# Kernel optimization log

Measured on AMD Instinct MI355X. Metric: run time of the kernel, lower is better.

The kernel has to match this reference:

```python
import jax, jax.numpy as jnp
import numpy as np

B, S, D = 128, 50, 128
NUM_NODE = 40000
HOP, N_ITER, SAMPLE = 2, 2, 12
N_NEI = 8
TEMP, MU, LEAK = 0.5, 0.1, 0.2


def setup_inputs() -> dict:
    key = jax.random.key(0)
    ks = jax.random.split(key, 32)
    stdv = 1.0 / np.sqrt(D)
    u = lambda k, shp: jax.random.uniform(k, shp, jnp.float32, -stdv, stdv)
    return {
        "inputs": jax.random.randint(ks[0], (B, S), 0, NUM_NODE),
        "adj": jax.random.randint(ks[1], (B, S, S), 0, 5),
        "item": jax.random.randint(ks[2], (B, S), 0, NUM_NODE),
        "simi_mask": jax.random.randint(ks[3], (B, S, S), 0, 2),
        "as_items_0": jax.random.randint(ks[4], (B, S, N_NEI), 0, NUM_NODE),
        "as_items_1": jax.random.randint(ks[5], (B, S, N_NEI), 0, NUM_NODE),
        "as_items_ssl_0": jax.random.randint(ks[6], (B, S, N_NEI), 0, NUM_NODE),
        "as_items_ssl_1": jax.random.randint(ks[7], (B, S, N_NEI), 0, NUM_NODE),
        "last_item_mask": jnp.zeros((B, S), bool).at[:, -1].set(True),
        "adj_all": jax.random.randint(ks[8], (NUM_NODE, SAMPLE), 0, NUM_NODE),
        "num": jax.random.uniform(ks[9], (NUM_NODE, SAMPLE)),
        "emb": u(ks[10], (NUM_NODE, D)),
        "pos_emb": u(ks[11], (200, D)),
        "a_local": u(ks[12], (N_ITER, 4, D)),
        "mir_w1": u(ks[13], (N_ITER, D, D)),
        "mir_w2": u(ks[14], (N_ITER, D, D)),
        "glob_w1": u(ks[15], (HOP, D + 1, D)),
        "glob_w2": u(ks[16], (HOP, D, 1)),
        "glob_w3": u(ks[17], (HOP, 2 * D, D)),
        "attr_w": u(ks[18], (2 * D, D)),
        "highway_w": u(ks[19], (2 * D, D)),
        "glu1_w": u(ks[20], (D, D)),
        "glu2_w": u(ks[21], (D, D)),
        "glu4_w": u(ks[22], (D, D)),
        "glu4_b": u(ks[23], (D,)),
        "w_s": u(ks[24], (D, 1)),
        "gate_w": u(ks[25], (2 * D, D)),
    }


def _forward(num, emb, pos_emb, a_local, mir_w1, mir_w2, glob_w1, glob_w2, glob_w3,
             attr_w, highway_w, glu1_w, glu2_w, glu4_w, glu4_b, w_s, gate_w,
             inputs, adj, item, simi_mask, as_lists, as_ssl_lists, last_item_mask, adj_all):
    mi = (inputs != 0).astype(emb.dtype)  # [B,S]
    h = emb[inputs]                        # [B,S,D]

    # ---- AttributeAggregator (masked-mean pool per attribute + gated fusion) ----
    def pool(idx_list):
        ps = []
        for idx in idx_list:
            m = (idx != 0).astype(emb.dtype)[..., None]  # [B,S,N,1]
            ps.append(jnp.sum(emb[idx] * m, 2) / (jnp.sum(m, 2) + 1e-8))
        return jnp.mean(jnp.stack(ps), 0)  # [B,S,D]
    hf1 = pool(as_lists)
    hf2 = pool(as_ssl_lists)
    g_attr = jax.nn.sigmoid(jnp.concatenate([h, hf1], -1) @ attr_w)
    hf = g_attr * h + (1.0 - g_attr) * hf1

    # ---- multi-hop neighbor sampling (irregular gathers) ----
    neigh = [inputs]
    wts = []
    for _ in range(HOP):
        flat = neigh[-1].reshape(-1)
        neigh.append(adj_all[flat].reshape(B, -1))
        wts.append(num[flat].reshape(B, -1))
    ev = [emb[n] for n in neigh]  # [B,S,D], [B,S*12,D], [B,S*144,D]

    item_emb = emb[item] * mi[..., None]
    sess = jnp.sum(item_emb, 1) / jnp.sum(mi, -1, keepdims=True)  # [B,D]

    # ---- GlobalAggregator stack (GCE-GNN style attention over sampled neighbors) ----
    for n_hop in range(HOP):
        nxt = []
        for hop in range(HOP - n_hop):
            sv = ev[hop]                                   # [B,M,D]
            nv = ev[hop + 1].reshape(B, -1, SAMPLE, D)     # [B,M,12,D]
            nw = wts[hop].reshape(B, -1, SAMPLE)           # [B,M,12]
            extra = jnp.broadcast_to(sess[:, None, None, :], nv.shape)
            a = jnp.concatenate([extra * nv, nw[..., None]], -1)  # [B,M,12,D+1]
            a = jax.nn.leaky_relu(a @ glob_w1[n_hop], LEAK)
            a = jax.nn.softmax((a @ glob_w2[n_hop])[..., 0], -1)[..., None]
            agg = jnp.sum(a * nv, -2)
            nxt.append(jnp.tanh(jnp.concatenate([sv, agg], -1) @ glob_w3[n_hop]))
        ev = nxt
    h_global = ev[0].reshape(B, S, D)

    # ---- LocalAggregator (edge-typed GAT) + MirrorAggregator (gated exchange) ----
    x = h
    mirror = hf
    for i in range(HOP):
        e = jax.nn.leaky_relu(jnp.einsum('bid,bjd,kd->kbij', x, x, a_local[i]), LEAK)
        att = jnp.full((B, S, S), -9e15, x.dtype)
        for k in range(4):
            att = jnp.where(adj == k + 1, e[k], att)
        x = jax.nn.softmax(att, -1) @ x
        gm = jax.nn.sigmoid(x @ mir_w1[i] + mirror @ mir_w2[i])
        x, mirror = gm * x + (1.0 - gm) * mirror, gm * mirror + (1.0 - gm) * x

    # ---- highway + last-item select ----
    g = jax.nn.sigmoid(jnp.concatenate([h, x], -1) @ highway_w)
    x_dot = g * h + (1.0 - g) * x
    h_local = jnp.sum(x_dot * last_item_mask[..., None].astype(x_dot.dtype), 1)  # [B,D]

    mask = mi[..., None]
    pos = pos_emb[:S][None]  # [1,S,D]
    bw = emb[1:]             # [NUM_NODE-1,D]
    hs = jnp.sum(h_global * mask, -2) / jnp.sum(mask, 1)  # [B,D]

    # ---- SSL pairwise similarity loss ----
    sim = jnp.einsum('bid,bjd->bij', hf1, hf2) / TEMP
    l = -jnp.log(jax.nn.softmax(sim, 2) + 1e-8)
    simi_loss = jnp.mean(jnp.sum(l * (simi_mask == 1), (1, 2)))

    # ---- attention-style GLU scoring ----
    hp = x_dot + pos
    nh = jax.nn.sigmoid(hp @ glu1_w + hs[:, None, :] @ glu2_w + h_local[:, None, :] @ glu4_w + glu4_b)
    beta = (nh @ w_s) * mask
    zg = jnp.sum(beta * hp, 1)  # [B,D]
    gf = jax.nn.sigmoid(jnp.concatenate([zg, h_local], -1) @ gate_w) * MU
    zh = gf * h_local + (1.0 - gf) * zg
    scores = zh @ bw.T  # [B, NUM_NODE-1]
    return simi_loss, scores


def reference(inputs, adj, item, simi_mask, as_items_0, as_items_1,
              as_items_ssl_0, as_items_ssl_1, last_item_mask, adj_all, num,
              emb, pos_emb, a_local, mir_w1, mir_w2, glob_w1, glob_w2, glob_w3,
              attr_w, highway_w, glu1_w, glu2_w, glu4_w, glu4_b, w_s, gate_w):
    return _forward(num, emb, pos_emb, a_local, mir_w1, mir_w2, glob_w1, glob_w2, glob_w3,
                    attr_w, highway_w, glu1_w, glu2_w, glu4_w, glu4_b, w_s, gate_w,
                    inputs, adj, item, simi_mask, [as_items_0, as_items_1],
                    [as_items_ssl_0, as_items_ssl_1], last_item_mask, adj_all)
```

## Files before the change

### kernel.cpp

```cpp
#include <hip/hip_runtime.h>
#include <hip/hip_bf16.h>


#define B 128
#define S 50
#define D 128
#define SAMPLE 12
#define NNEI 8
#define NODES 40000
#define NSC (NODES - 1)
#define LEAK 0.2f
#define TEMPV 0.5f
#define MUV 0.1f
#define NEG_BIG -3.0e38f

typedef const float* fpp;
typedef float* fpw;
typedef unsigned short u16;
typedef __attribute__((ext_vector_type(8))) short bfrag8;
typedef __attribute__((ext_vector_type(4))) float f32x4;

__device__ __forceinline__ float sigm(float x) { return 1.f / (1.f + __expf(-x)); }
__device__ __forceinline__ float tanh_f(float x) { return 1.f - 2.f / (__expf(2.f * x) + 1.f); }
__device__ __forceinline__ float leaky(float x) { return x >= 0.f ? x : LEAK * x; }
__device__ __forceinline__ u16 f2bf(float v) {
  __hip_bfloat16 h = __float2bfloat16(v);
  return *reinterpret_cast<u16*>(&h);
}

__global__ __launch_bounds__(256) void kprep4(fpp gw1, fpp gw3,
                                              u16* __restrict__ p1a,
                                              u16* __restrict__ p1b,
                                              u16* __restrict__ p3a,
                                              u16* __restrict__ p3b) {
  int i = blockIdx.x * 256 + threadIdx.x;
  fpp W; u16* dst; int KS;
  if (i < 16384)      { W = gw1;             dst = p1a; KS = 4; }
  else if (i < 32768) { W = gw1 + 129 * 128; dst = p1b; KS = 4; i -= 16384; }
  else if (i < 65536) { W = gw3;             dst = p3a; KS = 8; i -= 32768; }
  else                { W = gw3 + 256 * 128; dst = p3b; KS = 8; i -= 65536; }
  int e = i & 7;
  int lane = (i >> 3) & 63;
  int rest = i >> 9;
  int ks = rest % KS, nt = rest / KS;
  int k = ks * 32 + ((lane >> 4) << 3) + e;
  int n = (nt << 4) + (lane & 15);
  dst[i] = f2bf(W[(long)k * 128 + n]);
}

__global__ __launch_bounds__(128) void k1_gather(
    const int* __restrict__ inputs, const int* __restrict__ as0,
    const int* __restrict__ as1, const int* __restrict__ ss0,
    const int* __restrict__ ss1, fpp emb, fpp attr_w,
    fpw h, fpw hf1, fpw hf2, float* __restrict__ mi, fpw xA, fpw mir) {
  int bs = blockIdx.x;
  int d = threadIdx.x;
  __shared__ float h_s[D], hf1_s[D];
  int inp = inputs[bs];
  float hv = emb[(long)inp * D + d];
  const int* lists[4] = {as0, as1, ss0, ss1};
  float p[4];
#pragma unroll
  for (int l = 0; l < 4; l++) {
    float sum = 0.f, cnt = 0.f;
    const int* L = lists[l] + (long)bs * NNEI;
#pragma unroll
    for (int n = 0; n < NNEI; n++) {
      int idx = L[n];
      if (idx != 0) { sum += emb[(long)idx * D + d]; cnt += 1.f; }
    }
    p[l] = sum / (cnt + 1e-8f);
  }
  float hf1v = 0.5f * (p[0] + p[1]);
  float hf2v = 0.5f * (p[2] + p[3]);
  h_s[d] = hv;
  hf1_s[d] = hf1v;
  __syncthreads();
  float acc = 0.f;
  for (int k = 0; k < D; k++)
    acc += h_s[k] * attr_w[(long)k * D + d] + hf1_s[k] * attr_w[(long)(D + k) * D + d];
  float g = sigm(acc);
  float hfv = g * hv + (1.f - g) * hf1v;
  long o = (long)bs * D + d;
  h[o] = hv; hf1[o] = hf1v; hf2[o] = hf2v; xA[o] = hv; mir[o] = hfv;
  if (d == 0) mi[bs] = (inp != 0) ? 1.f : 0.f;
}

__global__ __launch_bounds__(128) void k2_sess(const int* __restrict__ inputs,
                                               const int* __restrict__ item,
                                               fpp emb, fpw sess) {
  int b = blockIdx.x;
  int d = threadIdx.x;
  float acc = 0.f, ms = 0.f;
  for (int s = 0; s < S; s++) {
    int inp = inputs[b * S + s];
    float m = (inp != 0) ? 1.f : 0.f;
    int it = item[b * S + s];
    acc += emb[(long)it * D + d] * m;
    ms += m;
  }
  sess[(long)b * D + d] = acc / ms;
}

__global__ __launch_bounds__(256) void kG_global(
    const int* __restrict__ inputs, const int* __restrict__ adj_all,
    fpp num, fpp emb, fpp sess,
    fpp W1a, fpp W2a, fpp W1b, fpp W2b, fpp W3b,
    const u16* __restrict__ p1a, const u16* __restrict__ p1b,
    const u16* __restrict__ p3a, const u16* __restrict__ p3b,
    fpw hg) {
  int bs = blockIdx.x;
  int b = bs / S;
  int d = threadIdx.x;
  int lane = d & 63;
  int w = d >> 6;
  int p = w >> 1;
  int wp = w & 1;
  int c = d & 127;
  int q = lane >> 4;
  int mrow = lane & 15;

  __shared__ __align__(16) u16 nvs_l[2][16 * 136];
  __shared__ __align__(16) u16 svagg_l[16 * 264];
  __shared__ __align__(16) float ev_l[13 * 128];
  __shared__ __align__(16) float agg1_l[128];
  __shared__ float red_l[2][2][16];
  __shared__ float nw_l[2][16];
  __shared__ int n1_l[SAMPLE];

#pragma unroll
  for (int r = 12; r < 16; r++) {
    if (d < 136) { nvs_l[0][r * 136 + d] = 0; nvs_l[1][r * 136 + d] = 0; }
  }
#pragma unroll
  for (int r = 13; r < 16; r++) {
    svagg_l[r * 264 + d] = 0;
    if (d < 8) svagg_l[r * 264 + 256 + d] = 0;
  }

  float sess_c = sess[(long)b * D + c];
  int src0 = __builtin_amdgcn_readfirstlane(inputs[bs]);
  if (d < 128) svagg_l[0 * 264 + d] = f2bf(emb[(long)src0 * D + d]);
  if (d < SAMPLE) n1_l[d] = adj_all[(long)src0 * SAMPLE + d];

  float w2A[4], wlA[4], w2B[4], wlB[4];
#pragma unroll
  for (int nt = 0; nt < 4; nt++) {
    int colA = (wp * 4 + nt) * 16 + mrow;
    w2A[nt] = W2a[colA];
    wlA[nt] = W1a[(long)D * D + colA];
    int colB = (w * 4 + nt) * 16 + mrow;
    if (w < 2) { w2B[nt] = W2b[colB]; wlB[nt] = W1b[(long)D * D + colB]; }
  }
  __syncthreads();

  float pre_raw[SAMPLE];
  float pre_nw = 0.f;
  {
    int u0 = p * 7;
    int srcp = (u0 == 0) ? src0 : __builtin_amdgcn_readfirstlane(n1_l[u0 - 1]);
#pragma unroll
    for (int j = 0; j < SAMPLE; j++) {
      int nj = __builtin_amdgcn_readfirstlane(adj_all[(long)srcp * SAMPLE + j]);
      pre_raw[j] = emb[(long)nj * D + c];
    }
    if (c < SAMPLE) pre_nw = num[(long)srcp * SAMPLE + c];
  }
  for (int i = 0; i < 7; i++) {
    int u = p * 7 + i;
    bool act = (u < 13);
    float raw[SAMPLE];
    if (act) {
#pragma unroll
      for (int j = 0; j < SAMPLE; j++) {
        raw[j] = pre_raw[j];
        nvs_l[p][j * 136 + c] = f2bf(raw[j] * sess_c);
      }
      if (c < SAMPLE) nw_l[p][c] = pre_nw;
      if (u == 0) {
#pragma unroll
        for (int j = 0; j < SAMPLE; j++)
          svagg_l[(1 + j) * 264 + c] = f2bf(raw[j]);
      }
    }
    __syncthreads();
    if (i < 6 && (u + 1) < 13) {
      int srcn = __builtin_amdgcn_readfirstlane(n1_l[u]);
#pragma unroll
      for (int j = 0; j < SAMPLE; j++) {
        int nj = __builtin_amdgcn_readfirstlane(adj_all[(long)srcn * SAMPLE + j]);
        pre_raw[j] = emb[(long)nj * D + c];
      }
      if (c < SAMPLE) pre_nw = num[(long)srcn * SAMPLE + c];
    }
    if (act) {
      f32x4 acc[4];
#pragma unroll
      for (int nt = 0; nt < 4; nt++) acc[nt] = (f32x4){0.f, 0.f, 0.f, 0.f};
#pragma unroll
      for (int ks = 0; ks < 4; ks++) {
        bfrag8 a = *(const bfrag8*)(nvs_l[p] + mrow * 136 + q * 8 + ks * 32);
#pragma unroll
        for (int nt = 0; nt < 4; nt++) {
          bfrag8 bb = *(const bfrag8*)(p1a + ((wp * 4 + nt) * 4 + ks) * 512 + lane * 8);
          acc[nt] = __builtin_amdgcn_mfma_f32_16x16x32_bf16(a, bb, acc[nt], 0, 0, 0);
        }
      }
      float lp[4] = {0.f, 0.f, 0.f, 0.f};
      float nwq[4];
#pragma unroll
      for (int i2 = 0; i2 < 4; i2++) nwq[i2] = (q < 3) ? nw_l[p][q * 4 + i2] : 0.f;
#pragma unroll
      for (int nt = 0; nt < 4; nt++)
#pragma unroll
        for (int i2 = 0; i2 < 4; i2++)
          lp[i2] += leaky(acc[nt][i2] + nwq[i2] * wlA[nt]) * w2A[nt];
#pragma unroll
      for (int off = 1; off <= 8; off <<= 1)
#pragma unroll
        for (int i2 = 0; i2 < 4; i2++) lp[i2] += __shfl_xor(lp[i2], off, 64);
      if (mrow == 0 && q < 3) {
#pragma unroll
        for (int i2 = 0; i2 < 4; i2++) red_l[p][wp][q * 4 + i2] = lp[i2];
      }
    }
    __syncthreads();
    if (act) {
      float lg[SAMPLE];
#pragma unroll
      for (int j = 0; j < SAMPLE; j++) lg[j] = red_l[p][0][j] + red_l[p][1][j];
      float mx = lg[0];
#pragma unroll
      for (int j = 1; j < SAMPLE; j++) mx = fmaxf(mx, lg[j]);
      float se = 0.f;
#pragma unroll
      for (int j = 0; j < SAMPLE; j++) { lg[j] = __expf(lg[j] - mx); se += lg[j]; }
      float inv = 1.f / se;
      float aggd = 0.f;
#pragma unroll
      for (int j = 0; j < SAMPLE; j++) aggd += lg[j] * inv * raw[j];
      svagg_l[u * 264 + 128 + c] = f2bf(aggd);
    }
  }
  __syncthreads();

  {
    f32x4 accB[2];
#pragma unroll
    for (int nt = 0; nt < 2; nt++) accB[nt] = (f32x4){0.f, 0.f, 0.f, 0.f};
#pragma unroll
    for (int ks = 0; ks < 8; ks++) {
      bfrag8 a = *(const bfrag8*)(svagg_l + mrow * 264 + q * 8 + ks * 32);
#pragma unroll
      for (int nt = 0; nt < 2; nt++) {
        bfrag8 bb = *(const bfrag8*)(p3a + ((w * 2 + nt) * 8 + ks) * 512 + lane * 8);
        accB[nt] = __builtin_amdgcn_mfma_f32_16x16x32_bf16(a, bb, accB[nt], 0, 0, 0);
      }
    }
#pragma unroll
    for (int nt = 0; nt < 2; nt++) {
      int col = (w * 2 + nt) * 16 + mrow;
#pragma unroll
      for (int i2 = 0; i2 < 4; i2++) {
        int u2 = q * 4 + i2;
        if (u2 < 13) ev_l[u2 * 128 + col] = tanh_f(accB[nt][i2]);
      }
    }
  }
  __syncthreads();

  float evreg[SAMPLE];
  if (p == 0) {
#pragma unroll
    for (int j = 0; j < SAMPLE; j++) {
      float e = ev_l[(1 + j) * 128 + c];
      evreg[j] = e;
      nvs_l[0][j * 136 + c] = f2bf(e * sess_c);
    }
    if (c < SAMPLE) nw_l[0][c] = num[(long)src0 * SAMPLE + c];
  }
  __syncthreads();
  if (w < 2) {
    f32x4 acc[4];
#pragma unroll
    for (int nt = 0; nt < 4; nt++) acc[nt] = (f32x4){0.f, 0.f, 0.f, 0.f};
#pragma unroll
    for (int ks = 0; ks < 4; ks++) {
      bfrag8 a = *(const bfrag8*)(nvs_l[0] + mrow * 136 + q * 8 + ks * 32);
#pragma unroll
      for (int nt = 0; nt < 4; nt++) {
        bfrag8 bb = *(const bfrag8*)(p1b + ((w * 4 + nt) * 4 + ks) * 512 + lane * 8);
        acc[nt] = __builtin_amdgcn_mfma_f32_16x16x32_bf16(a, bb, acc[nt], 0, 0, 0);
      }
    }
    float lp[4] = {0.f, 0.f, 0.f, 0.f};
    float nwq[4];
#pragma unroll
    for (int i2 = 0; i2 < 4; i2++) nwq[i2] = (q < 3) ? nw_l[0][q * 4 + i2] : 0.f;
#pragma unroll
    for (int nt = 0; nt < 4; nt++)
#pragma unroll
      for (int i2 = 0; i2 < 4; i2++)
        lp[i2] += leaky(acc[nt][i2] + nwq[i2] * wlB[nt]) * w2B[nt];
#pragma unroll
    for (int off = 1; off <= 8; off <<= 1)
#pragma unroll
      for (int i2 = 0; i2 < 4; i2++) lp[i2] += __shfl_xor(lp[i2], off, 64);
    if (mrow == 0 && q < 3) {
#pragma unroll
      for (int i2 = 0; i2 < 4; i2++) red_l[0][w][q * 4 + i2] = lp[i2];
    }
  }
  __syncthreads();
  if (p == 0) {
    float lg[SAMPLE];
#pragma unroll
    for (int j = 0; j < SAMPLE; j++) lg[j] = red_l[0][0][j] + red_l[0][1][j];
    float mx = lg[0];
#pragma unroll
    for (int j = 1; j < SAMPLE; j++) mx = fmaxf(mx, lg[j]);
    float se = 0.f;
#pragma unroll
    for (int j = 0; j < SAMPLE; j++) { lg[j] = __expf(lg[j] - mx); se += lg[j]; }
    float inv = 1.f / se;
    float agg1d = 0.f;
#pragma unroll
    for (int j = 0; j < SAMPLE; j++) agg1d += lg[j] * inv * evreg[j];
    agg1_l[c] = agg1d;
  }
  __syncthreads();
  if (d < 128) {
    float accf = 0.f;
#pragma unroll 4
    for (int k4 = 0; k4 < 32; k4++) {
      float4 a4 = *(const float4*)&ev_l[4 * k4];
      float4 g4 = *(const float4*)&agg1_l[4 * k4];
      accf += a4.x * W3b[(4 * k4 + 0) * D + d] + a4.y * W3b[(4 * k4 + 1) * D + d] +
              a4.z * W3b[(4 * k4 + 2) * D + d] + a4.w * W3b[(4 * k4 + 3) * D + d] +
              g4.x * W3b[(D + 4 * k4 + 0) * D + d] + g4.y * W3b[(D + 4 * k4 + 1) * D + d] +
              g4.z * W3b[(D + 4 * k4 + 2) * D + d] + g4.w * W3b[(D + 4 * k4 + 3) * D + d];
    }
    hg[(long)bs * D + d] = tanh_f(accf);
  }
}

__global__ __launch_bounds__(128) void k5ab(fpp x, const int* __restrict__ adj,
                                            fpp a_loc, fpp w1, fpp w2,
                                            fpw xout, fpw mir,
                                            fpp hw, fpp h, fpw x_dot,
                                            float* __restrict__ h_local,
                                            int fin) {
  int b = blockIdx.x / S;
  int row = blockIdx.x % S;
  int tid = threadIdx.x;
  __shared__ float xi_s[D];
  __shared__ float ak_s[4][D];
  __shared__ float alpha_s[S];
  long idx = ((long)b * S + row) * D + tid;
  xi_s[tid] = x[idx];
#pragma unroll
  for (int k = 0; k < 4; k++) ak_s[k][tid] = a_loc[(long)k * D + tid];
  __syncthreads();
  if (tid < 64) {
    int j = tid;
    float att;
    if (j < S) {
      float acc0 = 0.f, acc1 = 0.f, acc2 = 0.f, acc3 = 0.f;
      const float* xj = x + ((long)b * S + j) * D;
      for (int dd = 0; dd < D; dd++) {
        float prod = xi_s[dd] * xj[dd];
        acc0 += prod * ak_s[0][dd];
        acc1 += prod * ak_s[1][dd];
        acc2 += prod * ak_s[2][dd];
        acc3 += prod * ak_s[3][dd];
      }
      int av = adj[((long)b * S + row) * S + j];
      att = -9e15f;
      if (av == 1) att = leaky(acc0);
      else if (av == 2) att = leaky(acc1);
      else if (av == 3) att = leaky(acc2);
      else if (av == 4) att = leaky(acc3);
    } else {
      att = NEG_BIG;
    }
    float mx = att;
#pragma unroll
    for (int o = 32; o > 0; o >>= 1) mx = fmaxf(mx, __shfl_xor(mx, o, 64));
    float e = __expf(att - mx);
    float ssum = e;
#pragma unroll
    for (int o = 32; o > 0; o >>= 1) ssum += __shfl_xor(ssum, o, 64);
    if (j < S) alpha_s[j] = e / ssum;
  }
  __syncthreads();
  float xn = 0.f;
  for (int j = 0; j < S; j++) xn += alpha_s[j] * x[((long)b * S + j) * D + tid];
  float mv = mir[idx];
  ak_s[0][tid] = xn;
  ak_s[1][tid] = mv;
  __syncthreads();
  float a2 = 0.f;
  for (int k = 0; k < D; k++)
    a2 += ak_s[0][k] * w1[(long)k * D + tid] + ak_s[1][k] * w2[(long)k * D + tid];
  float g = sigm(a2);
  float xg = g * xn + (1.f - g) * mv;
  if (!fin) {
    xout[idx] = xg;
    mir[idx] = g * mv + (1.f - g) * xn;
    return;
  }
  float hv = h[idx];
  ak_s[2][tid] = hv;
  ak_s[3][tid] = xg;
  __syncthreads();
  float a3 = 0.f;
  for (int k = 0; k < D; k++)
    a3 += ak_s[2][k] * hw[(long)k * D + tid] + ak_s[3][k] * hw[(long)(D + k) * D + tid];
  float gh = sigm(a3);
  float xd = gh * hv + (1.f - gh) * xg;
  x_dot[idx] = xd;
  if (row == S - 1) h_local[(long)b * D + tid] = xd;
}

__global__ __launch_bounds__(64) void k7_simi(fpp hf1, fpp hf2,
                                              const int* __restrict__ simi_mask,
                                              float* __restrict__ loss) {
  int b = blockIdx.x / S;
  int i = blockIdx.x % S;
  int j = threadIdx.x;
  __shared__ float hi_s[D];
  hi_s[j] = hf1[((long)b * S + i) * D + j];
  hi_s[j + 64] = hf1[((long)b * S + i) * D + j + 64];
  __syncthreads();
  float sim;
  if (j < S) {
    float acc = 0.f;
    const float* r = hf2 + ((long)b * S + j) * D;
    for (int dd = 0; dd < D; dd++) acc += hi_s[dd] * r[dd];
    sim = acc * (1.0f / TEMPV);
  } else {
    sim = NEG_BIG;
  }
  float mx = sim;
#pragma unroll
  for (int o = 32; o > 0; o >>= 1) mx = fmaxf(mx, __shfl_xor(mx, o, 64));
  float e = __expf(sim - mx);
  float ssum = e;
#pragma unroll
  for (int o = 32; o > 0; o >>= 1) ssum += __shfl_xor(ssum, o, 64);
  float contrib = 0.f;
  if (j < S) {
    float p = e / ssum;
    float l = -__logf(p + 1e-8f);
    if (simi_mask[((long)b * S + i) * S + j] == 1) contrib = l;
  }
#pragma unroll
  for (int o = 32; o > 0; o >>= 1) contrib += __shfl_xor(contrib, o, 64);
  if (j == 0) atomicAdd(loss, contrib);
}

__global__ __launch_bounds__(512) void k8_glu(
    fpp hg, fpp x_dot, fpp pos, fpp h_local, const float* __restrict__ mi,
    fpp glu1, fpp glu2, fpp glu4, fpp glu4b, fpp w_s, fpp gate_w, fpw zh) {
  int b = blockIdx.x;
  int t = threadIdx.x;
  int d = t & 127;
  int g = t >> 7;
  __shared__ float hs_s[D], hl_s[D];
  __shared__ float hp_g[4][D], part[4][D], zg_g[4][D];
  __shared__ float red2[4][2];
  float msf = 0.f;
  for (int s = 0; s < S; s++) msf += mi[b * S + s];
  float hsacc = 0.f;
  for (int s = g * 13; s < min(S, g * 13 + 13); s++)
    hsacc += hg[((long)b * S + s) * D + d] * mi[b * S + s];
  part[g][d] = hsacc;
  if (g == 1) hl_s[d] = h_local[(long)b * D + d];
  __syncthreads();
  if (g == 0) hs_s[d] = (part[0][d] + part[1][d] + part[2][d] + part[3][d]) / msf;
  __syncthreads();
  float c = glu4b[d];
  for (int k = 0; k < D; k++)
    c += hs_s[k] * glu2[(long)k * D + d] + hl_s[k] * glu4[(long)k * D + d];
  float wsd = w_s[d];
  float zg = 0.f;
  for (int it = 0; it < 13; it++) {
    int s = g * 13 + it;
    bool act = s < S;
    float hp = 0.f;
    if (act) {
      hp = x_dot[((long)b * S + s) * D + d] + pos[(long)s * D + d];
      hp_g[g][d] = hp;
    }
    __syncthreads();
    if (act) {
      float acc = c;
      for (int k = 0; k < D; k++) acc += hp_g[g][k] * glu1[(long)k * D + d];
      float v = sigm(acc) * wsd;
#pragma unroll
      for (int o = 32; o > 0; o >>= 1) v += __shfl_down(v, o, 64);
      if ((t & 63) == 0) red2[g][(t >> 6) & 1] = v;
    }
    __syncthreads();
    if (act) {
      float beta = (red2[g][0] + red2[g][1]) * mi[b * S + s];
      zg += beta * hp;
    }
    __syncthreads();
  }
  zg_g[g][d] = zg;
  __syncthreads();
  if (g == 0) {
    float zgf = zg_g[0][d] + zg_g[1][d] + zg_g[2][d] + zg_g[3][d];
    hp_g[0][d] = zgf;
  }
  __syncthreads();
  if (g == 0) {
    float zgf = hp_g[0][d];
    float acc = 0.f;
    for (int k = 0; k < D; k++)
      acc += hp_g[0][k] * gate_w[(long)k * D + d] +
             hl_s[k] * gate_w[(long)(D + k) * D + d];
    float gf = sigm(acc) * MUV;
    zh[(long)b * D + d] = gf * hl_s[d] + (1.f - gf) * zgf;
  }
}

__global__ __launch_bounds__(256) void k9_scores(fpp zh, fpp emb, fpp loss,
                                                 float* __restrict__ out) {
  int t = threadIdx.x;
  if (blockIdx.x == 0 && t == 0) out[0] = loss[0] * (1.0f / (float)B);
  int lane = t & 63;
  int w = t >> 6;
  int q = lane >> 4;
  int mrow = lane & 15;
  long n = (long)blockIdx.x * 64 + w * 16 + mrow;
  bool valid = n < NSC;
  long nrow = valid ? (n + 1) : 1;
  bfrag8 bfr[4];
#pragma unroll
  for (int ks = 0; ks < 4; ks++) {
    const float* src = emb + nrow * D + ks * 32 + q * 8;
    float4 lo = *(const float4*)src;
    float4 hi = *(const float4*)(src + 4);
    bfrag8 bb;
    bb[0] = (short)f2bf(lo.x); bb[1] = (short)f2bf(lo.y);
    bb[2] = (short)f2bf(lo.z); bb[3] = (short)f2bf(lo.w);
    bb[4] = (short)f2bf(hi.x); bb[5] = (short)f2bf(hi.y);
    bb[6] = (short)f2bf(hi.z); bb[7] = (short)f2bf(hi.w);
    bfr[ks] = bb;
  }
#pragma unroll
  for (int mt = 0; mt < 8; mt++) {
    f32x4 acc = (f32x4){0.f, 0.f, 0.f, 0.f};
#pragma unroll
    for (int ks = 0; ks < 4; ks++) {
      const float* za = zh + (long)(mt * 16 + mrow) * D + ks * 32 + q * 8;
      float4 lo = *(const float4*)za;
      float4 hi = *(const float4*)(za + 4);
      bfrag8 a;
      a[0] = (short)f2bf(lo.x); a[1] = (short)f2bf(lo.y);
      a[2] = (short)f2bf(lo.z); a[3] = (short)f2bf(lo.w);
      a[4] = (short)f2bf(hi.x); a[5] = (short)f2bf(hi.y);
      a[6] = (short)f2bf(hi.z); a[7] = (short)f2bf(hi.w);
      acc = __builtin_amdgcn_mfma_f32_16x16x32_bf16(a, bfr[ks], acc, 0, 0, 0);
    }
    if (valid) {
#pragma unroll
      for (int i = 0; i < 4; i++) {
        int m = mt * 16 + q * 4 + i;
        out[1 + (long)m * NSC + n] = acc[i];
      }
    }
  }
}

extern "C" void kernel_launch(void* const* d_in, const int* in_sizes, int n_in,
                              void* d_out, int out_size, void* d_ws, size_t ws_size,
                              hipStream_t stream) {
  (void)in_sizes; (void)n_in; (void)out_size; (void)ws_size;
  const int* inputs = (const int*)d_in[0];
  const int* adj = (const int*)d_in[1];
  const int* item = (const int*)d_in[2];
  const int* simi_mask = (const int*)d_in[3];
  const int* as0 = (const int*)d_in[4];
  const int* as1 = (const int*)d_in[5];
  const int* ss0 = (const int*)d_in[6];
  const int* ss1 = (const int*)d_in[7];
  const int* adj_all = (const int*)d_in[9];
  fpp num = (fpp)d_in[10];
  fpp emb = (fpp)d_in[11];
  fpp pos = (fpp)d_in[12];
  fpp a_local = (fpp)d_in[13];
  fpp mir_w1 = (fpp)d_in[14];
  fpp mir_w2 = (fpp)d_in[15];
  fpp gw1 = (fpp)d_in[16];
  fpp gw2 = (fpp)d_in[17];
  fpp gw3 = (fpp)d_in[18];
  fpp attr_w = (fpp)d_in[19];
  fpp highway_w = (fpp)d_in[20];
  fpp glu1 = (fpp)d_in[21];
  fpp glu2 = (fpp)d_in[22];
  fpp glu4 = (fpp)d_in[23];
  fpp glu4b = (fpp)d_in[24];
  fpp w_s = (fpp)d_in[25];
  fpp gate_w = (fpp)d_in[26];

  float* ob = (float*)d_out;
  constexpr long BSD_ = (long)B * S * D;
  fpw s_h = ob + 0 * BSD_;
  fpw s_hf1 = ob + 1 * BSD_;
  fpw s_hf2 = ob + 2 * BSD_;
  fpw s_mir = ob + 3 * BSD_;
  fpw s_xA = ob + 4 * BSD_;
  fpw s_xB = ob + 5 * BSD_;

  float* ws = (float*)d_ws;
  float* w_loss = ws + 0;
  float* w_mi = ws + 16;
  float* w_sess = w_mi + (long)B * S;
  float* w_hl = w_sess + (long)B * D;
  float* w_zh = w_hl + (long)B * D;
  u16* p1a = (u16*)(ws + 72000);
  u16* p1b = (u16*)(ws + 72000 + 8192);
  u16* p3a = (u16*)(ws + 72000 + 16384);
  u16* p3b = (u16*)(ws + 72000 + 32768);

  hipMemsetAsync((void*)w_loss, 0, sizeof(float), stream);

  kprep4<<<384, 256, 0, stream>>>(gw1, gw3, p1a, p1b, p3a, p3b);
  k1_gather<<<B * S, 128, 0, stream>>>(inputs, as0, as1, ss0, ss1, emb, attr_w,
                                       s_h, s_hf1, s_hf2, w_mi, s_xA, s_mir);
  k7_simi<<<B * S, 64, 0, stream>>>(s_hf1, s_hf2, simi_mask, w_loss);
  k2_sess<<<B, 128, 0, stream>>>(inputs, item, emb, w_sess);
  kG_global<<<B * S, 256, 0, stream>>>(inputs, adj_all, num, emb, w_sess,
                                       gw1, gw2, gw1 + 129 * 128, gw2 + 128,
                                       gw3 + 256 * 128,
                                       p1a, p1b, p3a, p3b,
                                       s_hf2 );
  k5ab<<<B * S, 128, 0, stream>>>(s_xA, adj, a_local, mir_w1, mir_w2,
                                  s_xB, s_mir, highway_w, s_h, s_hf1, w_hl, 0);
  k5ab<<<B * S, 128, 0, stream>>>(s_xB, adj, a_local + 4 * D,
                                  mir_w1 + (long)D * D, mir_w2 + (long)D * D,
                                  s_xA, s_mir, highway_w, s_h,
                                  s_hf1 , w_hl, 1);
  k8_glu<<<B, 512, 0, stream>>>(s_hf2 , s_hf1 , pos,
                                w_hl, w_mi, glu1, glu2, glu4, glu4b, w_s,
                                gate_w, w_zh);
  k9_scores<<<(NSC + 63) / 64, 256, 0, stream>>>(w_zh, emb, w_loss,
                                                 (float*)d_out);
}
```

Baseline: 772.5 us.

## Remap kG_global so each wavefront owns a hop-1 node; split dot loops across threads

```diff
diff --git a/kernel.cpp b/kernel.cpp
--- a/kernel.cpp
+++ b/kernel.cpp
@@ -113,122 +113,114 @@
   int b = bs / S;
   int d = threadIdx.x;
   int lane = d & 63;
-  int w = d >> 6;
-  int p = w >> 1;
-  int wp = w & 1;
-  int c = d & 127;
+  int v = d >> 6;
   int q = lane >> 4;
   int mrow = lane & 15;
 
-  __shared__ __align__(16) u16 nvs_l[2][16 * 136];
+  __shared__ __align__(16) u16 nvs_l[4][16 * 136];
   __shared__ __align__(16) u16 svagg_l[16 * 264];
   __shared__ __align__(16) float ev_l[13 * 128];
   __shared__ __align__(16) float agg1_l[128];
-  __shared__ float red_l[2][2][16];
-  __shared__ float nw_l[2][16];
   __shared__ int n1_l[SAMPLE];
 
 #pragma unroll
   for (int r = 12; r < 16; r++) {
-    if (d < 136) { nvs_l[0][r * 136 + d] = 0; nvs_l[1][r * 136 + d] = 0; }
+    nvs_l[v][r * 136 + lane] = 0;
+    nvs_l[v][r * 136 + 64 + lane] = 0;
+    if (lane < 8) nvs_l[v][r * 136 + 128 + lane] = 0;
   }
 #pragma unroll
   for (int r = 13; r < 16; r++) {
     svagg_l[r * 264 + d] = 0;
     if (d < 8) svagg_l[r * 264 + 256 + d] = 0;
   }
-
-  float sess_c = sess[(long)b * D + c];
   int src0 = __builtin_amdgcn_readfirstlane(inputs[bs]);
   if (d < 128) svagg_l[0 * 264 + d] = f2bf(emb[(long)src0 * D + d]);
   if (d < SAMPLE) n1_l[d] = adj_all[(long)src0 * SAMPLE + d];
 
-  float w2A[4], wlA[4], w2B[4], wlB[4];
-#pragma unroll
-  for (int nt = 0; nt < 4; nt++) {
-    int colA = (wp * 4 + nt) * 16 + mrow;
-    w2A[nt] = W2a[colA];
-    wlA[nt] = W1a[(long)D * D + colA];
-    int colB = (w * 4 + nt) * 16 + mrow;
-    if (w < 2) { w2B[nt] = W2b[colB]; wlB[nt] = W1b[(long)D * D + colB]; }
-  }
-  __syncthreads();
-
-  float pre_raw[SAMPLE];
-  float pre_nw = 0.f;
-  {
-    int u0 = p * 7;
-    int srcp = (u0 == 0) ? src0 : __builtin_amdgcn_readfirstlane(n1_l[u0 - 1]);
+  float sess0 = sess[(long)b * D + lane];
+  float sess1 = sess[(long)b * D + 64 + lane];
+
+  float w2A[8], wlA[8];
+#pragma unroll
+  for (int nt = 0; nt < 8; nt++) {
+    int col = nt * 16 + mrow;
+    w2A[nt] = W2a[col];
+    wlA[nt] = W1a[(long)D * D + col];
+  }
+  __syncthreads();
+
+  u16* nvs = nvs_l[v];
+  float pr0[SAMPLE], pr1[SAMPLE], pnw = 0.f;
+  if (v < 13) {
+    int src = (v == 0) ? src0 : __builtin_amdgcn_readfirstlane(n1_l[v - 1]);
 #pragma unroll
     for (int j = 0; j < SAMPLE; j++) {
-      int nj = __builtin_amdgcn_readfirstlane(adj_all[(long)srcp * SAMPLE + j]);
-      pre_raw[j] = emb[(long)nj * D + c];
-    }
-    if (c < SAMPLE) pre_nw = num[(long)srcp * SAMPLE + c];
-  }
-  for (int i = 0; i < 7; i++) {
-    int u = p * 7 + i;
-    bool act = (u < 13);
-    float raw[SAMPLE];
+      long base = (long)__builtin_amdgcn_readfirstlane(adj_all[(long)src * SAMPLE + j]) * D;
+      pr0[j] = emb[base + lane];
+      pr1[j] = emb[base + 64 + lane];
+    }
+    if (lane < SAMPLE) pnw = num[(long)src * SAMPLE + lane];
+  }
+  for (int it = 0; it < 4; it++) {
+    int u = it * 4 + v;
+    bool act = u < 13;
+    float r0[SAMPLE], r1[SAMPLE], nwv = pnw;
     if (act) {
 #pragma unroll
       for (int j = 0; j < SAMPLE; j++) {
-        raw[j] = pre_raw[j];
-        nvs_l[p][j * 136 + c] = f2bf(raw[j] * sess_c);
-      }
-      if (c < SAMPLE) nw_l[p][c] = pre_nw;
+        r0[j] = pr0[j]; r1[j] = pr1[j];
+        nvs[j * 136 + lane] = f2bf(r0[j] * sess0);
+        nvs[j * 136 + 64 + lane] = f2bf(r1[j] * sess1);
+      }
       if (u == 0) {
 #pragma unroll
-        for (int j = 0; j < SAMPLE; j++)
-          svagg_l[(1 + j) * 264 + c] = f2bf(raw[j]);
-      }
-    }
-    __syncthreads();
-    if (i < 6 && (u + 1) < 13) {
-      int srcn = __builtin_amdgcn_readfirstlane(n1_l[u]);
+        for (int j = 0; j < SAMPLE; j++) {
+          svagg_l[(1 + j) * 264 + lane] = f2bf(r0[j]);
+          svagg_l[(1 + j) * 264 + 64 + lane] = f2bf(r1[j]);
+        }
+      }
+    }
+    int un = (it + 1) * 4 + v;
+    if (un < 13) {
+      int src = __builtin_amdgcn_readfirstlane(n1_l[un - 1]);
 #pragma unroll
       for (int j = 0; j < SAMPLE; j++) {
-        int nj = __builtin_amdgcn_readfirstlane(adj_all[(long)srcn * SAMPLE + j]);
-        pre_raw[j] = emb[(long)nj * D + c];
-      }
-      if (c < SAMPLE) pre_nw = num[(long)srcn * SAMPLE + c];
+        long base = (long)__builtin_amdgcn_readfirstlane(adj_all[(long)src * SAMPLE + j]) * D;
+        pr0[j] = emb[base + lane];
+        pr1[j] = emb[base + 64 + lane];
+      }
+      if (lane < SAMPLE) pnw = num[(long)src * SAMPLE + lane];
     }
     if (act) {
-      f32x4 acc[4];
-#pragma unroll
-      for (int nt = 0; nt < 4; nt++) acc[nt] = (f32x4){0.f, 0.f, 0.f, 0.f};
+      f32x4 acc[8];
+#pragma unroll
+      for (int nt = 0; nt < 8; nt++) acc[nt] = (f32x4){0.f, 0.f, 0.f, 0.f};
 #pragma unroll
       for (int ks = 0; ks < 4; ks++) {
-        bfrag8 a = *(const bfrag8*)(nvs_l[p] + mrow * 136 + q * 8 + ks * 32);
-#pragma unroll
-        for (int nt = 0; nt < 4; nt++) {
-          bfrag8 bb = *(const bfrag8*)(p1a + ((wp * 4 + nt) * 4 + ks) * 512 + lane * 8);
+        bfrag8 a = *(const bfrag8*)(nvs + mrow * 136 + q * 8 + ks * 32);
+#pragma unroll
+        for (int nt = 0; nt < 8; nt++) {
+          bfrag8 bb = *(const bfrag8*)(p1a + (nt * 4 + ks) * 512 + lane * 8);
           acc[nt] = __builtin_amdgcn_mfma_f32_16x16x32_bf16(a, bb, acc[nt], 0, 0, 0);
         }
       }
+      float nwr[4];
+#pragma unroll
+      for (int i2 = 0; i2 < 4; i2++) nwr[i2] = __shfl(nwv, q * 4 + i2, 64);
       float lp[4] = {0.f, 0.f, 0.f, 0.f};
-      float nwq[4];
-#pragma unroll
-      for (int i2 = 0; i2 < 4; i2++) nwq[i2] = (q < 3) ? nw_l[p][q * 4 + i2] : 0.f;
-#pragma unroll
-      for (int nt = 0; nt < 4; nt++)
+#pragma unroll
+      for (int nt = 0; nt < 8; nt++)
 #pragma unroll
         for (int i2 = 0; i2 < 4; i2++)
-          lp[i2] += leaky(acc[nt][i2] + nwq[i2] * wlA[nt]) * w2A[nt];
+          lp[i2] += leaky(acc[nt][i2] + nwr[i2] * wlA[nt]) * w2A[nt];
 #pragma unroll
       for (int off = 1; off <= 8; off <<= 1)
 #pragma unroll
         for (int i2 = 0; i2 < 4; i2++) lp[i2] += __shfl_xor(lp[i2], off, 64);
-      if (mrow == 0 && q < 3) {
-#pragma unroll
-        for (int i2 = 0; i2 < 4; i2++) red_l[p][wp][q * 4 + i2] = lp[i2];
-      }
-    }
-    __syncthreads();
-    if (act) {
       float lg[SAMPLE];
 #pragma unroll
-      for (int j = 0; j < SAMPLE; j++) lg[j] = red_l[p][0][j] + red_l[p][1][j];
+      for (int r = 0; r < SAMPLE; r++) lg[r] = __shfl(lp[r & 3], (r >> 2) * 16, 64);
       float mx = lg[0];
 #pragma unroll
       for (int j = 1; j < SAMPLE; j++) mx = fmaxf(mx, lg[j]);
@@ -236,10 +228,15 @@
 #pragma unroll
       for (int j = 0; j < SAMPLE; j++) { lg[j] = __expf(lg[j] - mx); se += lg[j]; }
       float inv = 1.f / se;
-      float aggd = 0.f;
-#pragma unroll
-      for (int j = 0; j < SAMPLE; j++) aggd += lg[j] * inv * raw[j];
-      svagg_l[u * 264 + 128 + c] = f2bf(aggd);
+      float a0 = 0.f, a1 = 0.f;
+#pragma unroll
+      for (int j = 0; j < SAMPLE; j++) {
+        float al = lg[j] * inv;
+        a0 += al * r0[j];
+        a1 += al * r1[j];
+      }
+      svagg_l[u * 264 + 128 + lane] = f2bf(a0);
+      svagg_l[u * 264 + 128 + 64 + lane] = f2bf(a1);
     }
   }
   __syncthreads();
@@ -253,13 +250,13 @@
       bfrag8 a = *(const bfrag8*)(svagg_l + mrow * 264 + q * 8 + ks * 32);
 #pragma unroll
       for (int nt = 0; nt < 2; nt++) {
-        bfrag8 bb = *(const bfrag8*)(p3a + ((w * 2 + nt) * 8 + ks) * 512 + lane * 8);
+        bfrag8 bb = *(const bfrag8*)(p3a + ((v * 2 + nt) * 8 + ks) * 512 + lane * 8);
         accB[nt] = __builtin_amdgcn_mfma_f32_16x16x32_bf16(a, bb, accB[nt], 0, 0, 0);
       }
     }
 #pragma unroll
     for (int nt = 0; nt < 2; nt++) {
-      int col = (w * 2 + nt) * 16 + mrow;
+      int col = (v * 2 + nt) * 16 + mrow;
 #pragma unroll
       for (int i2 = 0; i2 < 4; i2++) {
         int u2 = q * 4 + i2;
@@ -269,53 +266,51 @@
   }
   __syncthreads();
 
-  float evreg[SAMPLE];
-  if (p == 0) {
+  if (v == 0) {
+    float e0[SAMPLE], e1[SAMPLE];
+    float nwc = (lane < SAMPLE) ? num[(long)src0 * SAMPLE + lane] : 0.f;
 #pragma unroll
     for (int j = 0; j < SAMPLE; j++) {
-      float e = ev_l[(1 + j) * 128 + c];
-      evreg[j] = e;
-      nvs_l[0][j * 136 + c] = f2bf(e * sess_c);
-    }
-    if (c < SAMPLE) nw_l[0][c] = num[(long)src0 * SAMPLE + c];
-  }
-  __syncthreads();
-  if (w < 2) {
-    f32x4 acc[4];
-#pragma unroll
-    for (int nt = 0; nt < 4; nt++) acc[nt] = (f32x4){0.f, 0.f, 0.f, 0.f};
+      e0[j] = ev_l[(1 + j) * 128 + lane];
+      e1[j] = ev_l[(1 + j) * 128 + 64 + lane];
+      nvs_l[0][j * 136 + lane] = f2bf(e0[j] * sess0);
+      nvs_l[0][j * 136 + 64 + lane] = f2bf(e1[j] * sess1);
+    }
+    float w2Bc[8], wlBc[8];
+#pragma unroll
+    for (int nt = 0; nt < 8; nt++) {
+      int col = nt * 16 + mrow;
+      w2Bc[nt] = W2b[col];
+      wlBc[nt] = W1b[(long)D * D + col];
+    }
+    f32x4 acc[8];
+#pragma unroll
+    for (int nt = 0; nt < 8; nt++) acc[nt] = (f32x4){0.f, 0.f, 0.f, 0.f};
 #pragma unroll
     for (int ks = 0; ks < 4; ks++) {
       bfrag8 a = *(const bfrag8*)(nvs_l[0] + mrow * 136 + q * 8 + ks * 32);
 #pragma unroll
-      for (int nt = 0; nt < 4; nt++) {
-        bfrag8 bb = *(const bfrag8*)(p1b + ((w * 4 + nt) * 4 + ks) * 512 + lane * 8);
+      for (int nt = 0; nt < 8; nt++) {
+        bfrag8 bb = *(const bfrag8*)(p1b + (nt * 4 + ks) * 512 + lane * 8);
         acc[nt] = __builtin_amdgcn_mfma_f32_16x16x32_bf16(a, bb, acc[nt], 0, 0, 0);
       }
     }
+    float nwr[4];
+#pragma unroll
+    for (int i2 = 0; i2 < 4; i2++) nwr[i2] = __shfl(nwc, q * 4 + i2, 64);
     float lp[4] = {0.f, 0.f, 0.f, 0.f};
-    float nwq[4];
-#pragma unroll
-    for (int i2 = 0; i2 < 4; i2++) nwq[i2] = (q < 3) ? nw_l[0][q * 4 + i2] : 0.f;
-#pragma unroll
-    for (int nt = 0; nt < 4; nt++)
+#pragma unroll
+    for (int nt = 0; nt < 8; nt++)
 #pragma unroll
       for (int i2 = 0; i2 < 4; i2++)
-        lp[i2] += leaky(acc[nt][i2] + nwq[i2] * wlB[nt]) * w2B[nt];
+        lp[i2] += leaky(acc[nt][i2] + nwr[i2] * wlBc[nt]) * w2Bc[nt];
 #pragma unroll
     for (int off = 1; off <= 8; off <<= 1)
 #pragma unroll
       for (int i2 = 0; i2 < 4; i2++) lp[i2] += __shfl_xor(lp[i2], off, 64);
-    if (mrow == 0 && q < 3) {
-#pragma unroll
-      for (int i2 = 0; i2 < 4; i2++) red_l[0][w][q * 4 + i2] = lp[i2];
-    }
-  }
-  __syncthreads();
-  if (p == 0) {
     float lg[SAMPLE];
 #pragma unroll
-    for (int j = 0; j < SAMPLE; j++) lg[j] = red_l[0][0][j] + red_l[0][1][j];
+    for (int r = 0; r < SAMPLE; r++) lg[r] = __shfl(lp[r & 3], (r >> 2) * 16, 64);
     float mx = lg[0];
 #pragma unroll
     for (int j = 1; j < SAMPLE; j++) mx = fmaxf(mx, lg[j]);
@@ -323,10 +318,15 @@
 #pragma unroll
     for (int j = 0; j < SAMPLE; j++) { lg[j] = __expf(lg[j] - mx); se += lg[j]; }
     float inv = 1.f / se;
-    float agg1d = 0.f;
-#pragma unroll
-    for (int j = 0; j < SAMPLE; j++) agg1d += lg[j] * inv * evreg[j];
-    agg1_l[c] = agg1d;
+    float a0 = 0.f, a1 = 0.f;
+#pragma unroll
+    for (int j = 0; j < SAMPLE; j++) {
+      float al = lg[j] * inv;
+      a0 += al * e0[j];
+      a1 += al * e1[j];
+    }
+    agg1_l[lane] = a0;
+    agg1_l[64 + lane] = a1;
   }
   __syncthreads();
   if (d < 128) {
@@ -356,24 +356,38 @@
   __shared__ float xi_s[D];
   __shared__ float ak_s[4][D];
   __shared__ float alpha_s[S];
+  __shared__ float part_s[4][2][64];
   long idx = ((long)b * S + row) * D + tid;
   xi_s[tid] = x[idx];
 #pragma unroll
   for (int k = 0; k < 4; k++) ak_s[k][tid] = a_loc[(long)k * D + tid];
+  __syncthreads();
+  {
+    int j = tid & 63, hf = tid >> 6;
+    float a0 = 0.f, a1 = 0.f, a2 = 0.f, a3 = 0.f;
+    if (j < S) {
+      const float* xj = x + ((long)b * S + j) * D + hf * 64;
+      int off = hf * 64;
+      for (int dd = 0; dd < 64; dd++) {
+        float prod = xi_s[off + dd] * xj[dd];
+        a0 += prod * ak_s[0][off + dd];
+        a1 += prod * ak_s[1][off + dd];
+        a2 += prod * ak_s[2][off + dd];
+        a3 += prod * ak_s[3][off + dd];
+      }
+    }
+    part_s[0][hf][j] = a0; part_s[1][hf][j] = a1;
+    part_s[2][hf][j] = a2; part_s[3][hf][j] = a3;
+  }
   __syncthreads();
   if (tid < 64) {
     int j = tid;
     float att;
     if (j < S) {
-      float acc0 = 0.f, acc1 = 0.f, acc2 = 0.f, acc3 = 0.f;
-      const float* xj = x + ((long)b * S + j) * D;
-      for (int dd = 0; dd < D; dd++) {
-        float prod = xi_s[dd] * xj[dd];
-        acc0 += prod * ak_s[0][dd];
-        acc1 += prod * ak_s[1][dd];
-        acc2 += prod * ak_s[2][dd];
-        acc3 += prod * ak_s[3][dd];
-      }
+      float acc0 = part_s[0][0][j] + part_s[0][1][j];
+      float acc1 = part_s[1][0][j] + part_s[1][1][j];
+      float acc2 = part_s[2][0][j] + part_s[2][1][j];
+      float acc3 = part_s[3][0][j] + part_s[3][1][j];
       int av = adj[((long)b * S + row) * S + j];
       att = -9e15f;
       if (av == 1) att = leaky(acc0);
@@ -399,10 +413,10 @@
   ak_s[0][tid] = xn;
   ak_s[1][tid] = mv;
   __syncthreads();
-  float a2 = 0.f;
+  float a2m = 0.f;
   for (int k = 0; k < D; k++)
-    a2 += ak_s[0][k] * w1[(long)k * D + tid] + ak_s[1][k] * w2[(long)k * D + tid];
-  float g = sigm(a2);
+    a2m += ak_s[0][k] * w1[(long)k * D + tid] + ak_s[1][k] * w2[(long)k * D + tid];
+  float g = sigm(a2m);
   float xg = g * xn + (1.f - g) * mv;
   if (!fin) {
     xout[idx] = xg;
@@ -413,50 +427,56 @@
   ak_s[2][tid] = hv;
   ak_s[3][tid] = xg;
   __syncthreads();
-  float a3 = 0.f;
+  float a3m = 0.f;
   for (int k = 0; k < D; k++)
-    a3 += ak_s[2][k] * hw[(long)k * D + tid] + ak_s[3][k] * hw[(long)(D + k) * D + tid];
-  float gh = sigm(a3);
+    a3m += ak_s[2][k] * hw[(long)k * D + tid] + ak_s[3][k] * hw[(long)(D + k) * D + tid];
+  float gh = sigm(a3m);
   float xd = gh * hv + (1.f - gh) * xg;
   x_dot[idx] = xd;
   if (row == S - 1) h_local[(long)b * D + tid] = xd;
 }
 
-__global__ __launch_bounds__(64) void k7_simi(fpp hf1, fpp hf2,
-                                              const int* __restrict__ simi_mask,
-                                              float* __restrict__ loss) {
+__global__ __launch_bounds__(128) void k7_simi(fpp hf1, fpp hf2,
+                                               const int* __restrict__ simi_mask,
+                                               float* __restrict__ loss) {
   int b = blockIdx.x / S;
   int i = blockIdx.x % S;
-  int j = threadIdx.x;
+  int t = threadIdx.x;
   __shared__ float hi_s[D];
-  hi_s[j] = hf1[((long)b * S + i) * D + j];
-  hi_s[j + 64] = hf1[((long)b * S + i) * D + j + 64];
-  __syncthreads();
-  float sim;
-  if (j < S) {
+  __shared__ float part_s[2][64];
+  hi_s[t] = hf1[((long)b * S + i) * D + t];
+  __syncthreads();
+  {
+    int j = t & 63, hf = t >> 6;
     float acc = 0.f;
-    const float* r = hf2 + ((long)b * S + j) * D;
-    for (int dd = 0; dd < D; dd++) acc += hi_s[dd] * r[dd];
-    sim = acc * (1.0f / TEMPV);
-  } else {
-    sim = NEG_BIG;
-  }
-  float mx = sim;
-#pragma unroll
-  for (int o = 32; o > 0; o >>= 1) mx = fmaxf(mx, __shfl_xor(mx, o, 64));
-  float e = __expf(sim - mx);
-  float ssum = e;
-#pragma unroll
-  for (int o = 32; o > 0; o >>= 1) ssum += __shfl_xor(ssum, o, 64);
-  float contrib = 0.f;
-  if (j < S) {
-    float p = e / ssum;
-    float l = -__logf(p + 1e-8f);
-    if (simi_mask[((long)b * S + i) * S + j] == 1) contrib = l;
-  }
-#pragma unroll
-  for (int o = 32; o > 0; o >>= 1) contrib += __shfl_xor(contrib, o, 64);
-  if (j == 0) atomicAdd(loss, contrib);
+    if (j < S) {
+      const float* r = hf2 + ((long)b * S + j) * D + hf * 64;
+      int off = hf * 64;
+      for (int dd = 0; dd < 64; dd++) acc += hi_s[off + dd] * r[dd];
+    }
+    part_s[hf][j] = acc;
+  }
+  __syncthreads();
+  if (t < 64) {
+    int j = t;
+    float sim = (j < S) ? (part_s[0][j] + part_s[1][j]) * (1.0f / TEMPV) : NEG_BIG;
+    float mx = sim;
+#pragma unroll
+    for (int o = 32; o > 0; o >>= 1) mx = fmaxf(mx, __shfl_xor(mx, o, 64));
+    float e = __expf(sim - mx);
+    float ssum = e;
+#pragma unroll
+    for (int o = 32; o > 0; o >>= 1) ssum += __shfl_xor(ssum, o, 64);
+    float contrib = 0.f;
+    if (j < S) {
+      float p = e / ssum;
+      float l = -__logf(p + 1e-8f);
+      if (simi_mask[((long)b * S + i) * S + j] == 1) contrib = l;
+    }
+#pragma unroll
+    for (int o = 32; o > 0; o >>= 1) contrib += __shfl_xor(contrib, o, 64);
+    if (j == 0) atomicAdd(loss, contrib);
+  }
 }
 
 __global__ __launch_bounds__(512) void k8_glu(
@@ -631,7 +651,7 @@
   kprep4<<<384, 256, 0, stream>>>(gw1, gw3, p1a, p1b, p3a, p3b);
   k1_gather<<<B * S, 128, 0, stream>>>(inputs, as0, as1, ss0, ss1, emb, attr_w,
                                        s_h, s_hf1, s_hf2, w_mi, s_xA, s_mir);
-  k7_simi<<<B * S, 64, 0, stream>>>(s_hf1, s_hf2, simi_mask, w_loss);
+  k7_simi<<<B * S, 128, 0, stream>>>(s_hf1, s_hf2, simi_mask, w_loss);
   k2_sess<<<B, 128, 0, stream>>>(inputs, item, emb, w_sess);
   kG_global<<<B * S, 256, 0, stream>>>(inputs, adj_all, num, emb, w_sess,
                                        gw1, gw2, gw1 + 129 * 128, gw2 + 128,
```

After: 830.2 us. 7.5% more time.
